# Performance work log

Hardware: AMD Instinct MI355X
Metric: run time of the kernel (lower is better)

The kernel has to match this reference:

```python
import jax, jax.numpy as jnp
import numpy as np

B, T, D_IN, H1, H2, K = 16, 1024, 384, 1024, 1024, 9


def _l2normalize(w, axis):
    # matches F.normalize(w, dim=axis): w / max(||w||_2, 1e-12)
    n = jnp.sqrt(jnp.sum(w * w, axis=axis, keepdims=True))
    return w / jnp.maximum(n, 1e-12)


def _mish(x):
    return x * jnp.tanh(jax.nn.softplus(x))


def setup_inputs() -> dict:
    key = jax.random.key(0)
    ks = jax.random.split(key, 11)
    f32 = jnp.float32
    return {
        "input": jax.random.normal(ks[0], (B, T, D_IN), f32),
        "d_w": jax.random.normal(ks[1], (B, H1, 1, K), f32),
        "d_g": jax.random.normal(ks[2], (B, H1), f32),
        "d_b": jax.random.normal(ks[3], (B, H1), f32),
        "p_w": jax.random.normal(ks[4], (B, H1, H2, 1), f32),
        "p_g": jax.random.normal(ks[5], (B, H1), f32),
        "p_b": jax.random.normal(ks[6], (B, H2), f32),
        "w1_w": jax.random.normal(ks[7], (H1, D_IN), f32) * 0.05,
        "w1_b": jax.random.normal(ks[8], (H1,), f32) * 0.05,
        "w2_w": jax.random.normal(ks[9], (D_IN, H2), f32) * 0.05,
        "w2_b": jax.random.normal(ks[10], (D_IN,), f32) * 0.05,
    }


def reference(input, d_w, d_g, d_b, p_w, p_g, p_b, w1_w, w1_b, w2_w, w2_b):
    residual = input
    # w_1: 1x1 conv == per-position linear, then Mish (dropout = identity in eval)
    h = _mish(jnp.einsum('btc,hc->bth', input, w1_w) + w1_b)   # [B,T,H1]
    x = jnp.transpose(h, (0, 2, 1))                            # [B,H1,T]
    k = d_w.shape[-1]
    pad = (k - 1) // 2
    t = x.shape[-1]
    xp = jnp.pad(x, ((0, 0), (0, 0), (pad, pad)))              # [B,H1,T+2p]
    idx = jnp.arange(t)[:, None] + jnp.arange(k)[None, :]      # [T,K]
    xu = xp[:, :, idx]                                         # [B,H1,T,K] (unfold)
    # weight-normalized dynamic depthwise conv weights
    dwn = _l2normalize(d_w, axis=1) * d_g[:, :, None, None]    # [B,H1,1,K]
    # torch.einsum('bctk,bcwk->bct') with d_w expanded along w(=T): w is summed,
    # and every w-slice is identical, so the dot product picks up a factor of T.
    y = jnp.einsum('bctk,bck->bct', xu, dwn[:, :, 0, :]) * t   # [B,H1,T]
    y = y + d_b[:, :, None]
    # weight-normalized dynamic pointwise mix
    pwn = _l2normalize(p_w, axis=1) * p_g[:, :, None, None]    # [B,H1,H2,1]
    z = jnp.einsum('bct,bco->bot', y, pwn[..., 0])             # [B,H2,T]
    z = z + p_b[:, :, None]
    # w_2: 1x1 conv back to d_in, residual add
    out2 = jnp.einsum('bot,do->btd', z, w2_w) + w2_b           # [B,T,D_IN]
    return out2 + residual
```

## Files before the change

kernel.cpp:

```cpp
#include <hip/hip_runtime.h>

#define BCNT 16
#define TT 1024
#define DIN 384
#define H1 1024
#define H2 1024
#define KW 9

typedef __attribute__((ext_vector_type(8))) short bhalf8;
typedef __attribute__((ext_vector_type(4))) float f32x4;

typedef const __attribute__((address_space(1))) void* gas_ptr;
typedef __attribute__((address_space(3))) void* lds_ptr;

__device__ __forceinline__ float bf2f(unsigned short u) {
    return __uint_as_float(((unsigned int)u) << 16);
}
__device__ __forceinline__ unsigned short f2bf(float f) {
    unsigned int u = __float_as_uint(f);
    unsigned int r = (u + 0x7FFFu + ((u >> 16) & 1u)) >> 16;
    return (unsigned short)r;
}
__device__ __forceinline__ float mish_f(float x) {
    if (x > 20.f) return x;
    float u = __expf(x);
    float n = u * u + 2.f * u;
    return x * n / (n + 2.f);
}


__global__ __launch_bounds__(256) void k_cvt(const float* __restrict__ src,
                                             unsigned short* __restrict__ dst, int n4) {
    int i = blockIdx.x * 256 + threadIdx.x;
    if (i < n4) {
        float4 v = ((const float4*)src)[i];
        ushort4 o;
        o.x = f2bf(v.x); o.y = f2bf(v.y); o.z = f2bf(v.z); o.w = f2bf(v.w);
        ((ushort4*)dst)[i] = o;
    }
}

__global__ void k_norm_d(const float* __restrict__ d_w, float* __restrict__ norm_d) {
    int idx = blockIdx.x;
    int b = idx / KW, k = idx % KW;
    float s = 0.f;
    for (int c = threadIdx.x; c < H1; c += 256) {
        float v = d_w[((size_t)b * H1 + c) * KW + k];
        s += v * v;
    }
    __shared__ float red[256];
    red[threadIdx.x] = s; __syncthreads();
    for (int st = 128; st > 0; st >>= 1) {
        if (threadIdx.x < st) red[threadIdx.x] += red[threadIdx.x + st];
        __syncthreads();
    }
    if (threadIdx.x == 0) norm_d[idx] = sqrtf(red[0]);
}

__global__ void k_dwn(const float* __restrict__ d_w, const float* __restrict__ d_g,
                      const float* __restrict__ norm_d, float* __restrict__ dwn_s) {
    int i = blockIdx.x * 256 + threadIdx.x;
    int k = i % KW;
    int c = (i / KW) % H1;
    int b = i / (KW * H1);
    float n = fmaxf(norm_d[b * KW + k], 1e-12f);
    dwn_s[i] = d_w[i] / n * d_g[b * H1 + c] * (float)TT;
}

__global__ __launch_bounds__(256) void k_norm_p_part(const float* __restrict__ p_w,
                                                     float* __restrict__ part) {
    int o = blockIdx.y * 256 + threadIdx.x;
    int b = blockIdx.x, ch = blockIdx.z;
    float s = 0.f;
    for (int c = ch * 128; c < ch * 128 + 128; c++) {
        float v = p_w[((size_t)b * H1 + c) * H2 + o];
        s += v * v;
    }
    part[((size_t)(b * 8 + ch)) * H2 + o] = s;
}

__global__ __launch_bounds__(256) void k_norm_p_fin(const float* __restrict__ part,
                                                    float* __restrict__ inv_np) {
    int o = blockIdx.y * 256 + threadIdx.x;
    int b = blockIdx.x;
    float s = 0.f;
#pragma unroll
    for (int ch = 0; ch < 8; ch++) s += part[((size_t)(b * 8 + ch)) * H2 + o];
    inv_np[b * H2 + o] = 1.0f / fmaxf(sqrtf(s), 1e-12f);
}

__global__ __launch_bounds__(256) void k_tpw(const float* __restrict__ p_w,
                                             const float* __restrict__ inv_np,
                                             const float* __restrict__ p_g,
                                             unsigned short* __restrict__ pwT) {
    __shared__ float tile[32][33];
    int tx = threadIdx.x & 31, ty = threadIdx.x >> 5;
    int c0 = blockIdx.x * 32, o0 = blockIdx.y * 32, b = blockIdx.z;
#pragma unroll
    for (int j = 0; j < 4; j++)
        tile[ty + j * 8][tx] = p_w[((size_t)b * H1 + c0 + ty + j * 8) * H2 + o0 + tx];
    __syncthreads();
#pragma unroll
    for (int j = 0; j < 4; j++) {
        int o = o0 + ty + j * 8, c = c0 + tx;
        float v = tile[tx][ty + j * 8] * inv_np[b * H2 + o] * p_g[(size_t)b * H1 + c];
        pwT[((size_t)b * H2 + o) * H1 + c] = f2bf(v);
    }
}

__global__ __launch_bounds__(256) void k_conv(const unsigned short* __restrict__ h,
                                              const float* __restrict__ dwn_s,
                                              const float* __restrict__ d_b,
                                              unsigned short* __restrict__ y) {
    int tid = threadIdx.x;
    int c2 = blockIdx.y * 256 + tid;
    int c = c2 * 2;
    int t0 = blockIdx.x * 64;
    int b = blockIdx.z;
    const ushort2* hb = (const ushort2*)(h + (size_t)b * TT * H1);
    ushort2* yb = (ushort2*)(y + (size_t)b * TT * H1);
    float k0[KW], k1[KW];
#pragma unroll
    for (int i = 0; i < KW; i++) {
        k0[i] = dwn_s[((size_t)b * H1 + c) * KW + i];
        k1[i] = dwn_s[((size_t)b * H1 + c + 1) * KW + i];
    }
    float db0 = d_b[b * H1 + c], db1 = d_b[b * H1 + c + 1];
    float w0[KW], w1[KW];
#pragma unroll
    for (int i = 0; i < 8; i++) {
        int t = t0 - 4 + i;
        if (t >= 0 && t < TT) {
            ushort2 v = hb[(size_t)t * (H1 / 2) + c2];
            w0[i] = bf2f(v.x); w1[i] = bf2f(v.y);
        } else { w0[i] = 0.f; w1[i] = 0.f; }
    }
    for (int j = 0; j < 64; j++) {
        int t = t0 + j;
        int tl = t + 4;
        if (tl < TT) {
            ushort2 v = hb[(size_t)tl * (H1 / 2) + c2];
            w0[8] = bf2f(v.x); w1[8] = bf2f(v.y);
        } else { w0[8] = 0.f; w1[8] = 0.f; }
        float a0 = db0, a1 = db1;
#pragma unroll
        for (int i = 0; i < KW; i++) { a0 += k0[i] * w0[i]; a1 += k1[i] * w1[i]; }
        ushort2 o; o.x = f2bf(a0); o.y = f2bf(a1);
        yb[(size_t)t * (H1 / 2) + c2] = o;
#pragma unroll
        for (int i = 0; i < 8; i++) { w0[i] = w0[i + 1]; w1[i] = w1[i + 1]; }
    }
}

template <int MODE, int SWIZ>
__global__ __launch_bounds__(256) void gemm_nt(
    const unsigned short* __restrict__ A, const unsigned short* __restrict__ Bm,
    void* __restrict__ Cp, int Kdim, int lda, int ldb, int ldc,
    long sA, long sB, long sC,
    const float* __restrict__ bias, int biasStride,
    const unsigned short* __restrict__ residbf) {
    __shared__ __attribute__((aligned(16))) unsigned short Al[128 * 32];
    __shared__ __attribute__((aligned(16))) unsigned short Bl[128 * 32];

    const int tid = threadIdx.x;
    const int lane = tid & 63, wv = tid >> 6;

    int bx, by, bz;
    if constexpr (SWIZ) {
        int l = blockIdx.x;
        int xcd = l & 7, s = l >> 3;
        bz = xcd * 2 + (s >> 6);
        int u = s & 63;
        bx = u & 7; by = u >> 3;
    } else {
        bx = blockIdx.x; by = blockIdx.y; bz = blockIdx.z;
    }
    const int bm = bx * 128, bn = by * 128;

    const unsigned short* Ab = A + (size_t)sA * bz;
    const unsigned short* Bb = Bm + (size_t)sB * bz;

    const int rS = lane >> 2;
    const int cS = (lane & 3) * 8;

    const int wm = (wv >> 1) * 64, wn = (wv & 1) * 64;
    const int l16 = lane & 15, quad = lane >> 4;

    f32x4 acc[4][4];
#pragma unroll
    for (int i = 0; i < 4; i++)
#pragma unroll
        for (int j = 0; j < 4; j++)
#pragma unroll
            for (int r = 0; r < 4; r++) acc[i][j][r] = 0.f;

    const int ktiles = Kdim / 32;
    for (int kt = 0; kt < ktiles; ++kt) {
        const int kofs = kt * 32 + cS;
#pragma unroll
        for (int i = 0; i < 2; i++) {
            const int ch = wv + i * 4;
            const unsigned short* ga = Ab + (size_t)(bm + ch * 16 + rS) * lda + kofs;
            __builtin_amdgcn_global_load_lds((gas_ptr)ga, (lds_ptr)&Al[ch * 512], 16, 0, 0);
            const unsigned short* gb = Bb + (size_t)(bn + ch * 16 + rS) * ldb + kofs;
            __builtin_amdgcn_global_load_lds((gas_ptr)gb, (lds_ptr)&Bl[ch * 512], 16, 0, 0);
        }
        __syncthreads();

        bhalf8 af[4], bf[4];
#pragma unroll
        for (int mi = 0; mi < 4; mi++)
            af[mi] = *(const bhalf8*)&Al[(wm + mi * 16 + l16) * 32 + quad * 8];
#pragma unroll
        for (int ni = 0; ni < 4; ni++)
            bf[ni] = *(const bhalf8*)&Bl[(wn + ni * 16 + l16) * 32 + quad * 8];
#pragma unroll
        for (int mi = 0; mi < 4; mi++)
#pragma unroll
            for (int ni = 0; ni < 4; ni++)
                acc[mi][ni] = __builtin_amdgcn_mfma_f32_16x16x32_bf16(af[mi], bf[ni],
                                                                     acc[mi][ni], 0, 0, 0);
        __syncthreads();
    }

#pragma unroll
    for (int mi = 0; mi < 4; mi++)
#pragma unroll
        for (int ni = 0; ni < 4; ni++)
#pragma unroll
            for (int r = 0; r < 4; r++) {
                int gm = bm + wm + mi * 16 + quad * 4 + r;
                int gn = bn + wn + ni * 16 + l16;
                float v = acc[mi][ni][r];
                size_t cidx = (size_t)sC * bz + (size_t)gm * ldc + gn;
                if constexpr (MODE == 0) {
                    v = mish_f(v + bias[gn]);
                    ((unsigned short*)Cp)[cidx] = f2bf(v);
                } else if constexpr (MODE == 1) {
                    v += bias[(size_t)bz * biasStride + gn];
                    ((unsigned short*)Cp)[cidx] = f2bf(v);
                } else {
                    v += bias[gn] + bf2f(residbf[cidx]);
                    ((float*)Cp)[cidx] = v;
                }
            }
}


extern "C" void kernel_launch(void* const* d_in, const int* in_sizes, int n_in,
                              void* d_out, int out_size, void* d_ws, size_t ws_size,
                              hipStream_t stream) {
    const float* input = (const float*)d_in[0];
    const float* d_w   = (const float*)d_in[1];
    const float* d_g   = (const float*)d_in[2];
    const float* d_b   = (const float*)d_in[3];
    const float* p_w   = (const float*)d_in[4];
    const float* p_g   = (const float*)d_in[5];
    const float* p_b   = (const float*)d_in[6];
    const float* w1_w  = (const float*)d_in[7];
    const float* w1_b  = (const float*)d_in[8];
    const float* w2_w  = (const float*)d_in[9];
    const float* w2_b  = (const float*)d_in[10];
    float* out = (float*)d_out;

    char* ws = (char*)d_ws;
    size_t off = 0;
    auto alloc = [&](size_t bytes) {
        char* p = ws + off;
        off += (bytes + 255) & ~(size_t)255;
        return p;
    };
    float* norm_d        = (float*)alloc((size_t)BCNT * KW * 4);
    float* dwn_s         = (float*)alloc((size_t)BCNT * H1 * KW * 4);
    float* np_part       = (float*)alloc((size_t)BCNT * 8 * H2 * 4);
    float* inv_np        = (float*)alloc((size_t)BCNT * H2 * 4);
    unsigned short* inbf = (unsigned short*)alloc((size_t)BCNT * TT * DIN * 2);
    unsigned short* w1bf = (unsigned short*)alloc((size_t)H1 * DIN * 2);
    unsigned short* w2bf = (unsigned short*)alloc((size_t)DIN * H2 * 2);
    unsigned short* h    = (unsigned short*)alloc((size_t)BCNT * TT * H1 * 2);
    unsigned short* y    = (unsigned short*)alloc((size_t)BCNT * TT * H1 * 2);
    unsigned short* pwT  = (unsigned short*)alloc((size_t)BCNT * H2 * H1 * 2);
    unsigned short* zt   = (unsigned short*)alloc((size_t)BCNT * TT * H2 * 2);

    k_cvt<<<(BCNT * TT * DIN / 4 + 255) / 256, 256, 0, stream>>>(input, inbf, BCNT * TT * DIN / 4);
    k_cvt<<<(H1 * DIN / 4 + 255) / 256, 256, 0, stream>>>(w1_w, w1bf, H1 * DIN / 4);
    k_cvt<<<(DIN * H2 / 4 + 255) / 256, 256, 0, stream>>>(w2_w, w2bf, DIN * H2 / 4);

    k_norm_d<<<BCNT * KW, 256, 0, stream>>>(d_w, norm_d);
    k_dwn<<<(BCNT * H1 * KW) / 256, 256, 0, stream>>>(d_w, d_g, norm_d, dwn_s);
    k_norm_p_part<<<dim3(BCNT, H2 / 256, 8), 256, 0, stream>>>(p_w, np_part);
    k_norm_p_fin<<<dim3(BCNT, H2 / 256), 256, 0, stream>>>(np_part, inv_np);
    k_tpw<<<dim3(H1 / 32, H2 / 32, BCNT), 256, 0, stream>>>(p_w, inv_np, p_g, pwT);

    gemm_nt<0, 0><<<dim3(BCNT * TT / 128, H1 / 128, 1), 256, 0, stream>>>(
        inbf, w1bf, h, DIN, DIN, DIN, H1, 0, 0, 0, w1_b, 0, nullptr);

    k_conv<<<dim3(TT / 64, H1 / 512, BCNT), 256, 0, stream>>>(h, dwn_s, d_b, y);

    gemm_nt<1, 1><<<dim3(1024, 1, 1), 256, 0, stream>>>(
        y, pwT, zt, H1, H1, H1, H2, (long)TT * H1, (long)H2 * H1, (long)TT * H2, p_b, H2, nullptr);

    gemm_nt<2, 0><<<dim3(BCNT * TT / 128, DIN / 128, 1), 256, 0, stream>>>(
        zt, w2bf, out, H2, H2, H2, DIN, 0, 0, 0, w2_b, 0, inbf);
}
```

Measured before the change: 327.3 us.

## Retile GEMMs to 128x64 with swizzled LDS, fuse p_w norm into transpose

Result: no change. 321.7 us (-1.7%).

```diff
diff --git a/kernel.cpp b/kernel.cpp
--- a/kernel.cpp
+++ b/kernel.cpp
@@ -29,15 +29,25 @@
 }
 
 
-__global__ __launch_bounds__(256) void k_cvt(const float* __restrict__ src,
-                                             unsigned short* __restrict__ dst, int n4) {
+__global__ __launch_bounds__(256) void k_cvt3(
+    const float* __restrict__ s0, unsigned short* __restrict__ d0, int n0,
+    const float* __restrict__ s1, unsigned short* __restrict__ d1, int n1,
+    const float* __restrict__ s2, unsigned short* __restrict__ d2, int n2) {
     int i = blockIdx.x * 256 + threadIdx.x;
-    if (i < n4) {
-        float4 v = ((const float4*)src)[i];
-        ushort4 o;
-        o.x = f2bf(v.x); o.y = f2bf(v.y); o.z = f2bf(v.z); o.w = f2bf(v.w);
-        ((ushort4*)dst)[i] = o;
-    }
+    const float* s; unsigned short* d; int j = i;
+    if (i < n0) { s = s0; d = d0; }
+    else if ((j = i - n0) < n1) { s = s1; d = d1; }
+    else if ((j = i - n0 - n1) < n2) { s = s2; d = d2; }
+    else return;
+    float4 v = ((const float4*)s)[j];
+    ushort4 o;
+    o.x = f2bf(v.x); o.y = f2bf(v.y); o.z = f2bf(v.z); o.w = f2bf(v.w);
+    ((ushort4*)d)[j] = o;
+}
+
+__global__ __launch_bounds__(256) void k_zero(float* __restrict__ p, int n) {
+    int i = blockIdx.x * 256 + threadIdx.x;
+    if (i < n) p[i] = 0.f;
 }
 
 __global__ void k_norm_d(const float* __restrict__ d_w, float* __restrict__ norm_d) {
@@ -67,45 +77,41 @@
     dwn_s[i] = d_w[i] / n * d_g[b * H1 + c] * (float)TT;
 }
 
-__global__ __launch_bounds__(256) void k_norm_p_part(const float* __restrict__ p_w,
-                                                     float* __restrict__ part) {
-    int o = blockIdx.y * 256 + threadIdx.x;
-    int b = blockIdx.x, ch = blockIdx.z;
-    float s = 0.f;
-    for (int c = ch * 128; c < ch * 128 + 128; c++) {
-        float v = p_w[((size_t)b * H1 + c) * H2 + o];
-        s += v * v;
-    }
-    part[((size_t)(b * 8 + ch)) * H2 + o] = s;
-}
-
-__global__ __launch_bounds__(256) void k_norm_p_fin(const float* __restrict__ part,
-                                                    float* __restrict__ inv_np) {
-    int o = blockIdx.y * 256 + threadIdx.x;
-    int b = blockIdx.x;
-    float s = 0.f;
-#pragma unroll
-    for (int ch = 0; ch < 8; ch++) s += part[((size_t)(b * 8 + ch)) * H2 + o];
-    inv_np[b * H2 + o] = 1.0f / fmaxf(sqrtf(s), 1e-12f);
-}
-
-__global__ __launch_bounds__(256) void k_tpw(const float* __restrict__ p_w,
-                                             const float* __restrict__ inv_np,
-                                             const float* __restrict__ p_g,
-                                             unsigned short* __restrict__ pwT) {
+__global__ __launch_bounds__(256) void k_tpw2(const float* __restrict__ p_w,
+                                              const float* __restrict__ p_g,
+                                              unsigned short* __restrict__ pwTu,
+                                              float* __restrict__ sumsq) {
     __shared__ float tile[32][33];
+    __shared__ float red[8][32];
     int tx = threadIdx.x & 31, ty = threadIdx.x >> 5;
     int c0 = blockIdx.x * 32, o0 = blockIdx.y * 32, b = blockIdx.z;
-#pragma unroll
-    for (int j = 0; j < 4; j++)
-        tile[ty + j * 8][tx] = p_w[((size_t)b * H1 + c0 + ty + j * 8) * H2 + o0 + tx];
+    float s = 0.f;
+#pragma unroll
+    for (int j = 0; j < 4; j++) {
+        float v = p_w[((size_t)b * H1 + c0 + ty + j * 8) * H2 + o0 + tx];
+        tile[ty + j * 8][tx] = v;
+        s += v * v;
+    }
+    red[ty][tx] = s;
     __syncthreads();
+    if (ty == 0) {
+        float t = 0.f;
+#pragma unroll
+        for (int r = 0; r < 8; r++) t += red[r][tx];
+        atomicAdd(&sumsq[(size_t)b * H2 + o0 + tx], t);
+    }
 #pragma unroll
     for (int j = 0; j < 4; j++) {
         int o = o0 + ty + j * 8, c = c0 + tx;
-        float v = tile[tx][ty + j * 8] * inv_np[b * H2 + o] * p_g[(size_t)b * H1 + c];
-        pwT[((size_t)b * H2 + o) * H1 + c] = f2bf(v);
-    }
+        float v = tile[tx][ty + j * 8] * p_g[(size_t)b * H1 + c];
+        pwTu[((size_t)b * H2 + o) * H1 + c] = f2bf(v);
+    }
+}
+
+__global__ __launch_bounds__(256) void k_inv(const float* __restrict__ sumsq,
+                                             float* __restrict__ inv_np, int n) {
+    int i = blockIdx.x * 256 + threadIdx.x;
+    if (i < n) inv_np[i] = 1.0f / fmaxf(sqrtf(sumsq[i]), 1e-12f);
 }
 
 __global__ __launch_bounds__(256) void k_conv(const unsigned short* __restrict__ h,
@@ -153,14 +159,15 @@
 }
 
 template <int MODE, int SWIZ>
-__global__ __launch_bounds__(256) void gemm_nt(
+__global__ __launch_bounds__(128) void gemm_nt(
     const unsigned short* __restrict__ A, const unsigned short* __restrict__ Bm,
     void* __restrict__ Cp, int Kdim, int lda, int ldb, int ldc,
     long sA, long sB, long sC,
     const float* __restrict__ bias, int biasStride,
+    const float* __restrict__ scale,
     const unsigned short* __restrict__ residbf) {
     __shared__ __attribute__((aligned(16))) unsigned short Al[128 * 32];
-    __shared__ __attribute__((aligned(16))) unsigned short Bl[128 * 32];
+    __shared__ __attribute__((aligned(16))) unsigned short Bl[64 * 32];
 
     const int tid = threadIdx.x;
     const int lane = tid & 63, wv = tid >> 6;
@@ -169,22 +176,23 @@
     if constexpr (SWIZ) {
         int l = blockIdx.x;
         int xcd = l & 7, s = l >> 3;
-        bz = xcd * 2 + (s >> 6);
-        int u = s & 63;
+        bz = xcd * 2 + (s >> 7);
+        int u = s & 127;
         bx = u & 7; by = u >> 3;
     } else {
         bx = blockIdx.x; by = blockIdx.y; bz = blockIdx.z;
     }
-    const int bm = bx * 128, bn = by * 128;
+    const int bm = bx * 128, bn = by * 64;
 
     const unsigned short* Ab = A + (size_t)sA * bz;
     const unsigned short* Bb = Bm + (size_t)sB * bz;
 
     const int rS = lane >> 2;
-    const int cS = (lane & 3) * 8;
-
-    const int wm = (wv >> 1) * 64, wn = (wv & 1) * 64;
+    const int cS = (((lane & 3) ^ ((rS >> 1) & 3)) & 3) * 8;
+
+    const int wm = wv * 64;
     const int l16 = lane & 15, quad = lane >> 4;
+    const int fr = (l16 >> 1) & 3;
 
     f32x4 acc[4][4];
 #pragma unroll
@@ -198,10 +206,14 @@
     for (int kt = 0; kt < ktiles; ++kt) {
         const int kofs = kt * 32 + cS;
 #pragma unroll
-        for (int i = 0; i < 2; i++) {
-            const int ch = wv + i * 4;
+        for (int i = 0; i < 4; i++) {
+            const int ch = i * 2 + wv;
             const unsigned short* ga = Ab + (size_t)(bm + ch * 16 + rS) * lda + kofs;
             __builtin_amdgcn_global_load_lds((gas_ptr)ga, (lds_ptr)&Al[ch * 512], 16, 0, 0);
+        }
+#pragma unroll
+        for (int i = 0; i < 2; i++) {
+            const int ch = i * 2 + wv;
             const unsigned short* gb = Bb + (size_t)(bn + ch * 16 + rS) * ldb + kofs;
             __builtin_amdgcn_global_load_lds((gas_ptr)gb, (lds_ptr)&Bl[ch * 512], 16, 0, 0);
         }
@@ -210,10 +222,10 @@
         bhalf8 af[4], bf[4];
 #pragma unroll
         for (int mi = 0; mi < 4; mi++)
-            af[mi] = *(const bhalf8*)&Al[(wm + mi * 16 + l16) * 32 + quad * 8];
+            af[mi] = *(const bhalf8*)&Al[(wm + mi * 16 + l16) * 32 + ((quad ^ fr) & 3) * 8];
 #pragma unroll
         for (int ni = 0; ni < 4; ni++)
-            bf[ni] = *(const bhalf8*)&Bl[(wn + ni * 16 + l16) * 32 + quad * 8];
+            bf[ni] = *(const bhalf8*)&Bl[(ni * 16 + l16) * 32 + ((quad ^ fr) & 3) * 8];
 #pragma unroll
         for (int mi = 0; mi < 4; mi++)
 #pragma unroll
@@ -230,14 +242,15 @@
 #pragma unroll
             for (int r = 0; r < 4; r++) {
                 int gm = bm + wm + mi * 16 + quad * 4 + r;
-                int gn = bn + wn + ni * 16 + l16;
+                int gn = bn + ni * 16 + l16;
                 float v = acc[mi][ni][r];
                 size_t cidx = (size_t)sC * bz + (size_t)gm * ldc + gn;
                 if constexpr (MODE == 0) {
                     v = mish_f(v + bias[gn]);
                     ((unsigned short*)Cp)[cidx] = f2bf(v);
                 } else if constexpr (MODE == 1) {
-                    v += bias[(size_t)bz * biasStride + gn];
+                    size_t si = (size_t)bz * biasStride + gn;
+                    v = v * scale[si] + bias[si];
                     ((unsigned short*)Cp)[cidx] = f2bf(v);
                 } else {
                     v += bias[gn] + bf2f(residbf[cidx]);
@@ -272,34 +285,35 @@
     };
     float* norm_d        = (float*)alloc((size_t)BCNT * KW * 4);
     float* dwn_s         = (float*)alloc((size_t)BCNT * H1 * KW * 4);
-    float* np_part       = (float*)alloc((size_t)BCNT * 8 * H2 * 4);
+    float* sumsq         = (float*)alloc((size_t)BCNT * H2 * 4);
     float* inv_np        = (float*)alloc((size_t)BCNT * H2 * 4);
     unsigned short* inbf = (unsigned short*)alloc((size_t)BCNT * TT * DIN * 2);
     unsigned short* w1bf = (unsigned short*)alloc((size_t)H1 * DIN * 2);
     unsigned short* w2bf = (unsigned short*)alloc((size_t)DIN * H2 * 2);
     unsigned short* h    = (unsigned short*)alloc((size_t)BCNT * TT * H1 * 2);
     unsigned short* y    = (unsigned short*)alloc((size_t)BCNT * TT * H1 * 2);
-    unsigned short* pwT  = (unsigned short*)alloc((size_t)BCNT * H2 * H1 * 2);
+    unsigned short* pwTu = (unsigned short*)alloc((size_t)BCNT * H2 * H1 * 2);
     unsigned short* zt   = (unsigned short*)alloc((size_t)BCNT * TT * H2 * 2);
 
-    k_cvt<<<(BCNT * TT * DIN / 4 + 255) / 256, 256, 0, stream>>>(input, inbf, BCNT * TT * DIN / 4);
-    k_cvt<<<(H1 * DIN / 4 + 255) / 256, 256, 0, stream>>>(w1_w, w1bf, H1 * DIN / 4);
-    k_cvt<<<(DIN * H2 / 4 + 255) / 256, 256, 0, stream>>>(w2_w, w2bf, DIN * H2 / 4);
-
+    const int n4_in = BCNT * TT * DIN / 4, n4_w1 = H1 * DIN / 4, n4_w2 = DIN * H2 / 4;
+    k_cvt3<<<(n4_in + n4_w1 + n4_w2 + 255) / 256, 256, 0, stream>>>(
+        input, inbf, n4_in, w1_w, w1bf, n4_w1, w2_w, w2bf, n4_w2);
+
+    k_zero<<<(BCNT * H2 + 255) / 256, 256, 0, stream>>>(sumsq, BCNT * H2);
     k_norm_d<<<BCNT * KW, 256, 0, stream>>>(d_w, norm_d);
     k_dwn<<<(BCNT * H1 * KW) / 256, 256, 0, stream>>>(d_w, d_g, norm_d, dwn_s);
-    k_norm_p_part<<<dim3(BCNT, H2 / 256, 8), 256, 0, stream>>>(p_w, np_part);
-    k_norm_p_fin<<<dim3(BCNT, H2 / 256), 256, 0, stream>>>(np_part, inv_np);
-    k_tpw<<<dim3(H1 / 32, H2 / 32, BCNT), 256, 0, stream>>>(p_w, inv_np, p_g, pwT);
-
-    gemm_nt<0, 0><<<dim3(BCNT * TT / 128, H1 / 128, 1), 256, 0, stream>>>(
-        inbf, w1bf, h, DIN, DIN, DIN, H1, 0, 0, 0, w1_b, 0, nullptr);
+    k_tpw2<<<dim3(H1 / 32, H2 / 32, BCNT), 256, 0, stream>>>(p_w, p_g, pwTu, sumsq);
+    k_inv<<<(BCNT * H2 + 255) / 256, 256, 0, stream>>>(sumsq, inv_np, BCNT * H2);
+
+    gemm_nt<0, 0><<<dim3(BCNT * TT / 128, H1 / 64, 1), 128, 0, stream>>>(
+        inbf, w1bf, h, DIN, DIN, DIN, H1, 0, 0, 0, w1_b, 0, nullptr, nullptr);
 
     k_conv<<<dim3(TT / 64, H1 / 512, BCNT), 256, 0, stream>>>(h, dwn_s, d_b, y);
 
-    gemm_nt<1, 1><<<dim3(1024, 1, 1), 256, 0, stream>>>(
-        y, pwT, zt, H1, H1, H1, H2, (long)TT * H1, (long)H2 * H1, (long)TT * H2, p_b, H2, nullptr);
-
-    gemm_nt<2, 0><<<dim3(BCNT * TT / 128, DIN / 128, 1), 256, 0, stream>>>(
-        zt, w2bf, out, H2, H2, H2, DIN, 0, 0, 0, w2_b, 0, inbf);
-}
+    gemm_nt<1, 1><<<dim3(2048, 1, 1), 128, 0, stream>>>(
+        y, pwTu, zt, H1, H1, H1, H2, (long)TT * H1, (long)H2 * H1, (long)TT * H2,
+        p_b, H2, inv_np, nullptr);
+
+    gemm_nt<2, 0><<<dim3(BCNT * TT / 128, DIN / 64, 1), 128, 0, stream>>>(
+        zt, w2bf, out, H2, H2, H2, DIN, 0, 0, 0, w2_b, 0, nullptr, inbf);
+}
```
